# Performance work log

Hardware: AMD Instinct MI355X
Metric: run time of the kernel (lower is better)

## Reference

```python
import jax, jax.numpy as jnp
import numpy as np

H, CH, PQ, PV = 12, 16, 4, 8
C_S = 384
INF, EPS = 1e5, 1e-8
PT_W = -0.5


def setup_inputs() -> dict:
    key = jax.random.key(0)
    ks = jax.random.split(key, 20)
    B, C, N = 1, 8, 256
    s = jax.random.normal(ks[0], (B, C, N, C_S), jnp.float32)
    z = jax.random.normal(ks[1], (B, C, N, N, 8), jnp.float32)
    A = jax.random.normal(ks[2], (B, C, N, 3, 3), jnp.float32)
    rot = jnp.linalg.qr(A)[0]  # proper orthonormal frames
    trans = jax.random.normal(ks[3], (B, C, N, 3), jnp.float32) * 10.0
    mask = jnp.ones((B, C, N), jnp.float32)
    w = lambda k, i, o: jax.random.normal(k, (i, o), jnp.float32) * 0.02
    hc = H * CH
    return {
        's': s, 'z': z, 'rot': rot, 'trans': trans, 'mask': mask,
        'wq': w(ks[4], C_S, hc), 'bq': jnp.zeros((hc,)),
        'wkv': w(ks[5], C_S, 2 * hc), 'bkv': jnp.zeros((2 * hc,)),
        'g_gamma': jnp.ones((C_S,)), 'g_beta': jnp.zeros((C_S,)),
        'wgq': w(ks[6], C_S, hc), 'bgq': jnp.zeros((hc,)),
        'wgk': w(ks[7], C_S, hc), 'bgk': jnp.zeros((hc,)),
        'wqp': w(ks[8], C_S, H * PQ * 3), 'bqp': jnp.zeros((H * PQ * 3,)),
        'wkvp': w(ks[9], C_S, H * (PQ + PV) * 3), 'bkvp': jnp.zeros((H * (PQ + PV) * 3,)),
        'head_weights': jnp.full((H,), 0.5413248538970947, jnp.float32),  # softplus^-1(1)
        'wdist': w(ks[10], 1, H), 'bdist': jnp.zeros((H,)),
        'wout': w(ks[11], H * (CH + 4 * PV), C_S), 'bout': jnp.zeros((C_S,)),
    }


def _forward(s, z, rot, trans, mask, wq, bq, wkv, bkv, g_gamma, g_beta,
             wgq, bgq, wgk, bgk, wqp, bqp, wkvp, bkvp, head_weights,
             wdist, bdist, wout, bout):
    B, C, N, _ = s.shape
    q = (s @ wq + bq).reshape(B, C, N, H, CH)
    kv = (s @ wkv + bkv).reshape(B, C, N, H, 2 * CH)
    k, v = kv[..., :CH], kv[..., CH:]
    scale = (1.0 / (3 * CH)) ** 0.5
    a = jnp.einsum('bcihd,bcjhd->bchij', q, k) * scale  # [B,C,H,N,N]
    # global feature: mean over conformations, LayerNorm, QK bias
    s_g = s.mean(axis=-3)
    mu = s_g.mean(-1, keepdims=True)
    var = ((s_g - mu) ** 2).mean(-1, keepdims=True)
    s_gn = (s_g - mu) / jnp.sqrt(var + 1e-5) * g_gamma + g_beta
    g_q = (s_gn @ wgq + bgq).reshape(B, N, H, CH)
    g_k = (s_gn @ wgk + bgk).reshape(B, N, H, CH)
    a = a + jnp.einsum('bihd,bjhd->bhij', g_q, g_k)[:, None] * scale
    # invariant point attention term
    def to_pts(raw, P):
        pts = jnp.stack(jnp.split(raw, 3, axis=-1), axis=-1)  # [B,C,N,H*P,3]
        pts = jnp.einsum('bcnij,bcnpj->bcnpi', rot, pts) + trans[..., None, :]
        return pts.reshape(B, C, N, H, P, 3)
    q_pts = to_pts(s @ wqp + bqp, PQ)
    kv_pts = to_pts(s @ wkvp + bkvp, PQ + PV)
    k_pts, v_pts = kv_pts[..., :PQ, :], kv_pts[..., PQ:, :]
    diff2 = jnp.sum((q_pts[:, :, :, None] - k_pts[:, :, None]) ** 2, axis=-1)  # [B,C,N,N,H,PQ]
    hw = jax.nn.softplus(head_weights) * (1.0 / (3 * (PQ * 9.0 / 2))) ** 0.5
    pt_att = jnp.sum(diff2 * hw[:, None], axis=-1) * PT_W  # [B,C,N,N,H]
    a = a + jnp.moveaxis(pt_att, -1, -3)
    # mask
    sq_mask = mask[..., :, None] * mask[..., None, :]
    a = a + (INF * (sq_mask - 1.0))[..., None, :, :]
    # distance bias (torch uses a raw .view -> reshape, not transpose)
    dist = jnp.sqrt(jnp.sum((trans[..., :, None, :] - trans[..., None, :, :]) ** 2, axis=-1))
    db = dist[..., None] * wdist[0] + bdist  # [B,C,N,N,H]
    a = a + db.reshape(B, C, H, N, N)
    a = jax.nn.softmax(a, axis=-1)
    o = jnp.einsum('bchij,bcjhd->bcihd', a, v).reshape(B, C, N, H * CH)
    o_pt = jnp.einsum('bchij,bcjhpd->bcihpd', a, v_pts)  # [B,C,N,H,PV,3]
    o_pt = jnp.einsum('bcnji,bcnhpj->bcnhpi', rot, o_pt - trans[:, :, :, None, None, :])
    o_pt_norm = jnp.sqrt(jnp.sum(o_pt ** 2, axis=-1) + EPS).reshape(B, C, N, H * PV)
    o_pt_f = o_pt.reshape(B, C, N, H * PV, 3)
    feat = jnp.concatenate([o, o_pt_f[..., 0], o_pt_f[..., 1], o_pt_f[..., 2], o_pt_norm], axis=-1)
    return feat @ wout + bout, a


def reference(s, z, rot, trans, mask, wq, bq, wkv, bkv, g_gamma, g_beta,
              wgq, bgq, wgk, bgk, wqp, bqp, wkvp, bkvp, head_weights,
              wdist, bdist, wout, bout):
    return _forward(s, z, rot, trans, mask, wq, bq, wkv, bkv, g_gamma, g_beta,
                    wgq, bgq, wgk, bgk, wqp, bqp, wkvp, bkvp, head_weights,
                    wdist, bdist, wout, bout)
```

## Files before the change

### kernel.cpp

```cpp
#include <hip/hip_runtime.h>
#include <math.h>

#define NRES 256
#define CDIM 8
#define HNUM 12
#define CS   384

typedef __attribute__((ext_vector_type(8))) short bf16x8;
typedef __attribute__((ext_vector_type(4))) float f32x4;
typedef unsigned short ushort_t;

static __device__ __forceinline__ unsigned short f2bf(float x) {
    unsigned int u = __float_as_uint(x);
    unsigned int r = (u + 0x7fffu + ((u >> 16) & 1u)) >> 16;
    return (unsigned short)r;
}
static __device__ __forceinline__ float bf2f(unsigned short h) {
    return __uint_as_float(((unsigned int)h) << 16);
}

__global__ __launch_bounds__(256) void convert_kernel(
    const float* __restrict__ s,
    const float* __restrict__ wq, const float* __restrict__ bq,
    const float* __restrict__ wkv, const float* __restrict__ bkv,
    const float* __restrict__ wqp, const float* __restrict__ bqp,
    const float* __restrict__ wkvp, const float* __restrict__ bkvp,
    const float* __restrict__ wgq, const float* __restrict__ bgq,
    const float* __restrict__ wgk, const float* __restrict__ bgk,
    const float* __restrict__ wout,
    ushort_t* __restrict__ s_bf, ushort_t* __restrict__ wt_bf,
    ushort_t* __restrict__ wtg_bf, float* __restrict__ pbias,
    float* __restrict__ gbias,
    ushort_t* __restrict__ wo_hi, ushort_t* __restrict__ wo_lo)
{
    const int idx = blockIdx.x*256 + threadIdx.x;
    const int NS   = 2048*384;
    const int NWT  = 384*1152;
    const int NWTG = 384*384;
    const int NWO  = 576*384;
    if (idx < NS) {
        s_bf[idx] = f2bf(s[idx]);
    } else if (idx < NS + NWT) {
        const int t = idx - NS;
        const int k = t / 1152, vc = t - k*1152;
        const float* w; int C, lc;
        if (vc < 192)      { w = wq;   C = 192; lc = vc; }
        else if (vc < 576) { w = wkv;  C = 384; lc = vc - 192; }
        else if (vc < 720) { w = wqp;  C = 144; lc = vc - 576; }
        else               { w = wkvp; C = 432; lc = vc - 720; }
        wt_bf[(size_t)vc*384 + k] = f2bf(w[(size_t)k*C + lc]);
    } else if (idx < NS + NWT + NWTG) {
        const int t = idx - NS - NWT;
        const int k = t / 384, vc = t - k*384;
        const float val = (vc < 192) ? wgq[(size_t)k*192 + vc]
                                     : wgk[(size_t)k*192 + vc - 192];
        wtg_bf[(size_t)vc*384 + k] = f2bf(val);
    } else if (idx < NS + NWT + NWTG + 1152) {
        const int i = idx - NS - NWT - NWTG;
        float b;
        if (i < 192)      b = bq[i];
        else if (i < 576) b = bkv[i - 192];
        else if (i < 720) b = bqp[i - 576];
        else              b = bkvp[i - 720];
        pbias[i] = b;
    } else if (idx < NS + NWT + NWTG + 1152 + 384) {
        const int i = idx - NS - NWT - NWTG - 1152;
        gbias[i] = (i < 192) ? bgq[i] : bgk[i - 192];
    } else if (idx < NS + NWT + NWTG + 1536 + NWO) {
        const int t = idx - NS - NWT - NWTG - 1536;
        const int k = t / 384, n = t - k*384;
        const float wv = wout[t];
        const ushort_t hi = f2bf(wv);
        wo_hi[(size_t)n*576 + k] = hi;
        wo_lo[(size_t)n*576 + k] = f2bf(wv - bf2f(hi));
    }
}

__global__ __launch_bounds__(256) void proj_mfma_kernel(
    const ushort_t* __restrict__ s_bf, const ushort_t* __restrict__ wt_bf,
    const float* __restrict__ pbias,
    float* __restrict__ qo, float* __restrict__ ko, float* __restrict__ vo,
    float* __restrict__ rawp)
{
    const int blk = blockIdx.x;
    const int rt = blk / 18, ct = blk - rt*18;
    const int r0 = rt * 64, c0 = ct * 64;
    const int tid = threadIdx.x;
    const int wave = tid >> 6, lane = tid & 63;
    const int wrow = wave >> 1, wcol = wave & 1;
    const int m0 = r0 + wrow*32, n0 = c0 + wcol*32;
    const int qd = lane >> 4, lr = lane & 15;

    f32x4 acc00 = {0,0,0,0}, acc01 = {0,0,0,0}, acc10 = {0,0,0,0}, acc11 = {0,0,0,0};

    const ushort_t* a0p = s_bf  + (size_t)(m0 + lr)*384 + qd*8;
    const ushort_t* a1p = a0p + 16*384;
    const ushort_t* b0p = wt_bf + (size_t)(n0 + lr)*384 + qd*8;
    const ushort_t* b1p = b0p + 16*384;

    #pragma unroll
    for (int kk = 0; kk < 384; kk += 32) {
        const bf16x8 a0 = *(const bf16x8*)(a0p + kk);
        const bf16x8 a1 = *(const bf16x8*)(a1p + kk);
        const bf16x8 b0 = *(const bf16x8*)(b0p + kk);
        const bf16x8 b1 = *(const bf16x8*)(b1p + kk);
        acc00 = __builtin_amdgcn_mfma_f32_16x16x32_bf16(a0, b0, acc00, 0, 0, 0);
        acc01 = __builtin_amdgcn_mfma_f32_16x16x32_bf16(a0, b1, acc01, 0, 0, 0);
        acc10 = __builtin_amdgcn_mfma_f32_16x16x32_bf16(a1, b0, acc10, 0, 0, 0);
        acc11 = __builtin_amdgcn_mfma_f32_16x16x32_bf16(a1, b1, acc11, 0, 0, 0);
    }

    #pragma unroll
    for (int mt = 0; mt < 2; ++mt) {
        #pragma unroll
        for (int nt = 0; nt < 2; ++nt) {
            const f32x4 av = (mt==0) ? (nt==0 ? acc00 : acc01)
                                     : (nt==0 ? acc10 : acc11);
            const int col = n0 + nt*16 + lr;
            const float bb = pbias[col];
            #pragma unroll
            for (int reg = 0; reg < 4; ++reg) {
                const int row = m0 + mt*16 + qd*4 + reg;
                const float val = av[reg] + bb;
                if (col < 192) {
                    qo[(size_t)row*192 + col] = val;
                } else if (col < 576) {
                    const int lc = col - 192, h = lc >> 5, rm = lc & 31;
                    if (rm < 16) ko[(size_t)row*192 + h*16 + rm] = val;
                    else         vo[(size_t)row*192 + h*16 + rm - 16] = val;
                } else {
                    rawp[(size_t)row*576 + col - 576] = val;
                }
            }
        }
    }
}

__global__ __launch_bounds__(256) void pt_transform_kernel(
    const float* __restrict__ rawp, const float* __restrict__ rot,
    const float* __restrict__ trans,
    float* __restrict__ qpo, float* __restrict__ kpo, float* __restrict__ vpo)
{
    const int t = blockIdx.x*256 + threadIdx.x;
    const int row = t / 192;
    const int p = t - row*192;
    const float* R = rot + (size_t)row*9;
    const float* T = trans + (size_t)row*3;
    const float* base = rawp + (size_t)row*576;
    float x, y, z;
    if (p < 48) { x = base[p];       y = base[48+p];  z = base[96+p]; }
    else { const int pk = p-48; x = base[144+pk]; y = base[288+pk]; z = base[432+pk]; }
    const float px = R[0]*x + R[1]*y + R[2]*z + T[0];
    const float py = R[3]*x + R[4]*y + R[5]*z + T[1];
    const float pz = R[6]*x + R[7]*y + R[8]*z + T[2];
    if (p < 48) {
        float* o = qpo + (size_t)row*144 + p*3;
        o[0]=px; o[1]=py; o[2]=pz;
    } else {
        const int pk = p-48, h = pk/12, pp = pk - h*12;
        if (pp < 4) { float* o = kpo + (size_t)row*144 + (h*4+pp)*3;     o[0]=px; o[1]=py; o[2]=pz; }
        else        { float* o = vpo + (size_t)row*288 + (h*8+(pp-4))*3; o[0]=px; o[1]=py; o[2]=pz; }
    }
}

__global__ __launch_bounds__(256) void ln_kernel(
    const float* __restrict__ s, const float* __restrict__ g_gamma,
    const float* __restrict__ g_beta, ushort_t* __restrict__ sgn_bf)
{
    const int n = blockIdx.x;
    const int tid = threadIdx.x;
    __shared__ float sg[CS];
    __shared__ float red[256];

    for (int d = tid; d < CS; d += 256) {
        float acc = 0.f;
        for (int c = 0; c < CDIM; ++c) acc += s[((size_t)c*NRES+n)*CS + d];
        sg[d] = acc * (1.0f/CDIM);
    }
    __syncthreads();

    float lsum = 0.f;
    for (int d = tid; d < CS; d += 256) lsum += sg[d];
    red[tid] = lsum; __syncthreads();
    for (int st = 128; st > 0; st >>= 1) { if (tid < st) red[tid] += red[tid+st]; __syncthreads(); }
    const float mean = red[0] * (1.0f/CS);
    __syncthreads();

    float lvar = 0.f;
    for (int d = tid; d < CS; d += 256) { float df = sg[d]-mean; lvar += df*df; }
    red[tid] = lvar; __syncthreads();
    for (int st = 128; st > 0; st >>= 1) { if (tid < st) red[tid] += red[tid+st]; __syncthreads(); }
    const float var = red[0] * (1.0f/CS);
    __syncthreads();

    const float inv = rsqrtf(var + 1e-5f);
    for (int d = tid; d < CS; d += 256)
        sgn_bf[(size_t)n*CS + d] = f2bf((sg[d]-mean)*inv*g_gamma[d] + g_beta[d]);
}

__global__ __launch_bounds__(256) void ggemm_mfma_kernel(
    const ushort_t* __restrict__ sgn_bf, const ushort_t* __restrict__ wtg_bf,
    const float* __restrict__ gbias,
    float* __restrict__ gqo, float* __restrict__ gko)
{
    const int blk = blockIdx.x;
    const int rt = blk / 6, ct = blk - rt*6;
    const int r0 = rt * 64, c0 = ct * 64;
    const int tid = threadIdx.x;
    const int wave = tid >> 6, lane = tid & 63;
    const int wrow = wave >> 1, wcol = wave & 1;
    const int m0 = r0 + wrow*32, n0 = c0 + wcol*32;
    const int qd = lane >> 4, lr = lane & 15;

    f32x4 acc00 = {0,0,0,0}, acc01 = {0,0,0,0}, acc10 = {0,0,0,0}, acc11 = {0,0,0,0};

    const ushort_t* a0p = sgn_bf + (size_t)(m0 + lr)*384 + qd*8;
    const ushort_t* a1p = a0p + 16*384;
    const ushort_t* b0p = wtg_bf + (size_t)(n0 + lr)*384 + qd*8;
    const ushort_t* b1p = b0p + 16*384;

    #pragma unroll
    for (int kk = 0; kk < 384; kk += 32) {
        const bf16x8 a0 = *(const bf16x8*)(a0p + kk);
        const bf16x8 a1 = *(const bf16x8*)(a1p + kk);
        const bf16x8 b0 = *(const bf16x8*)(b0p + kk);
        const bf16x8 b1 = *(const bf16x8*)(b1p + kk);
        acc00 = __builtin_amdgcn_mfma_f32_16x16x32_bf16(a0, b0, acc00, 0, 0, 0);
        acc01 = __builtin_amdgcn_mfma_f32_16x16x32_bf16(a0, b1, acc01, 0, 0, 0);
        acc10 = __builtin_amdgcn_mfma_f32_16x16x32_bf16(a1, b0, acc10, 0, 0, 0);
        acc11 = __builtin_amdgcn_mfma_f32_16x16x32_bf16(a1, b1, acc11, 0, 0, 0);
    }

    #pragma unroll
    for (int mt = 0; mt < 2; ++mt) {
        #pragma unroll
        for (int nt = 0; nt < 2; ++nt) {
            const f32x4 av = (mt==0) ? (nt==0 ? acc00 : acc01)
                                     : (nt==0 ? acc10 : acc11);
            const int col = n0 + nt*16 + lr;
            const float bb = gbias[col];
            #pragma unroll
            for (int reg = 0; reg < 4; ++reg) {
                const int row = m0 + mt*16 + qd*4 + reg;
                const float val = av[reg] + bb;
                if (col < 192) gqo[(size_t)row*192 + col]       = val;
                else           gko[(size_t)row*192 + col - 192] = val;
            }
        }
    }
}

__global__ __launch_bounds__(256) void attn_mfma_kernel(
    const float* __restrict__ q, const float* __restrict__ k,
    const float* __restrict__ q_pts, const float* __restrict__ k_pts,
    const float* __restrict__ g_q, const float* __restrict__ g_k,
    const float* __restrict__ trans, const float* __restrict__ mask,
    const float* __restrict__ head_weights, const float* __restrict__ wdist,
    const float* __restrict__ bdist, float* __restrict__ a_out)
{
    const int blk  = blockIdx.x;
    const int half = blk & 1;
    const int ch   = blk >> 1;
    const int h    = ch % HNUM;
    const int c    = ch / HNUM;
    const int i0   = half * 128;
    const int tid  = threadIdx.x;

    __shared__ ushort_t Bsh[256*96];
    __shared__ ushort_t Ash[128*96];
    __shared__ float dsh[12*256];
    __shared__ float tsh[768];
    __shared__ float msh[256];
    __shared__ float kn_sh[256];
    __shared__ float qn_sh[128];
    __shared__ float wdsh[12], bdsh[12];
    __shared__ float cpart[96];
    __shared__ float censh[3];

    for (int t = tid; t < 768; t += 256) tsh[t] = trans[(size_t)c*768 + t];
    msh[tid] = mask[c*NRES + tid];
    if (tid < 12) { wdsh[tid] = wdist[tid]; bdsh[tid] = bdist[tid]; }
    __syncthreads();

    if (tid < 96) {
        const int coord = tid % 3, chunk = tid / 3;
        float sv = 0.f;
        for (int e = 0; e < 8; ++e) sv += tsh[(chunk*8+e)*3 + coord];
        cpart[tid] = sv;
    }
    __syncthreads();
    if (tid < 3) {
        float sv = 0.f;
        for (int e = 0; e < 32; ++e) sv += cpart[e*3 + tid];
        censh[tid] = sv * (1.0f/256.0f);
    }
    __syncthreads();

    const float s54   = 0.13608276348795434f;
    const float scale = 0.14433756729740643f;
    const float hwv = 0.5f * logf(1.0f + expf(head_weights[h])) * s54;
    const float sh  = sqrtf(2.0f * hwv);
    const float cx = censh[0], cy = censh[1], cz = censh[2];

    {
        const int j = tid;
        const float* kr  = k    + ((size_t)c*NRES + j)*192 + h*16;
        const float* gkr = g_k  + (size_t)j*192 + h*16;
        const float* kpr = k_pts+ ((size_t)c*NRES + j)*144 + h*12;
        ushort_t* br = &Bsh[j*96];
        #pragma unroll
        for (int e = 0; e < 16; ++e) br[e]    = f2bf(kr[e]);
        #pragma unroll
        for (int e = 0; e < 16; ++e) br[16+e] = f2bf(gkr[e]);
        float kn = 0.f;
        #pragma unroll
        for (int e = 0; e < 12; ++e) {
            const float cen = (e%3==0) ? cx : ((e%3==1) ? cy : cz);
            const float kp = kpr[e] - cen;
            kn += kp*kp;
            const float sp = sh * kp;
            const ushort_t hi = f2bf(sp);
            br[32+e] = hi;
            br[44+e] = f2bf(sp - bf2f(hi));
            br[56+e] = hi;
        }
        #pragma unroll
        for (int e = 68; e < 96; ++e) br[e] = 0;
        kn_sh[j] = hwv * kn;
    }

    if (tid < 128) {
        const int il = i0 + tid;
        const float* qr  = q    + ((size_t)c*NRES + il)*192 + h*16;
        const float* gqr = g_q  + (size_t)il*192 + h*16;
        const float* qpr = q_pts+ ((size_t)c*NRES + il)*144 + h*12;
        ushort_t* ar = &Ash[tid*96];
        #pragma unroll
        for (int e = 0; e < 16; ++e) ar[e]    = f2bf(scale*qr[e]);
        #pragma unroll
        for (int e = 0; e < 16; ++e) ar[16+e] = f2bf(scale*gqr[e]);
        float qn = 0.f;
        #pragma unroll
        for (int e = 0; e < 12; ++e) {
            const float cen = (e%3==0) ? cx : ((e%3==1) ? cy : cz);
            const float qp = qpr[e] - cen;
            qn += qp*qp;
            const float sp = sh * qp;
            const ushort_t hi = f2bf(sp);
            ar[32+e] = hi;
            ar[44+e] = hi;
            ar[56+e] = f2bf(sp - bf2f(hi));
        }
        #pragma unroll
        for (int e = 68; e < 96; ++e) ar[e] = 0;
        qn_sh[tid] = hwv * qn;
    }

    const int Fmin = h*65536 + i0*256;
    const int iibase = Fmin / 3072;
    const int NI = (Fmin + 127*256 + 255)/3072 - iibase + 1;
    for (int idx = tid; idx < NI*256; idx += 256) {
        const int e = idx >> 8, jj = idx & 255;
        const int ia = iibase + e;
        const float dx = tsh[ia*3+0] - tsh[jj*3+0];
        const float dy = tsh[ia*3+1] - tsh[jj*3+1];
        const float dz = tsh[ia*3+2] - tsh[jj*3+2];
        dsh[idx] = sqrtf(dx*dx + dy*dy + dz*dz);
    }
    __syncthreads();

    const int wave = tid >> 6, lane = tid & 63;
    const int qd = lane >> 4, lr = lane & 15;

    for (int g = 0; g < 2; ++g) {
        const int m0 = wave*32 + g*16;
        const ushort_t* ap = &Ash[(m0 + lr)*96 + qd*8];
        const bf16x8 af0 = *(const bf16x8*)(ap);
        const bf16x8 af1 = *(const bf16x8*)(ap + 32);
        const bf16x8 af2 = *(const bf16x8*)(ap + 64);

        f32x4 acc[16];
        #pragma unroll
        for (int t = 0; t < 16; ++t) {
            const ushort_t* bp = &Bsh[(t*16 + lr)*96 + qd*8];
            f32x4 a = {0.f,0.f,0.f,0.f};
            a = __builtin_amdgcn_mfma_f32_16x16x32_bf16(af0, *(const bf16x8*)(bp),      a, 0, 0, 0);
            a = __builtin_amdgcn_mfma_f32_16x16x32_bf16(af1, *(const bf16x8*)(bp + 32), a, 0, 0, 0);
            a = __builtin_amdgcn_mfma_f32_16x16x32_bf16(af2, *(const bf16x8*)(bp + 64), a, 0, 0, 0);
            acc[t] = a;
        }

        const int ibase = m0 + qd*4;
        float qn_r[4], mb_r[4];
        int F0_[4];
        #pragma unroll
        for (int r = 0; r < 4; ++r) {
            const int il = i0 + ibase + r;
            qn_r[r] = qn_sh[ibase + r];
            mb_r[r] = 100000.0f * msh[il];
            F0_[r]  = h*65536 + il*256;
        }

        float mx[4] = {-1e30f,-1e30f,-1e30f,-1e30f};
        #pragma unroll
        for (int t = 0; t < 16; ++t) {
            const int j = t*16 + lr;
            const float knj = kn_sh[j];
            const float mj  = msh[j];
            #pragma unroll
            for (int r = 0; r < 4; ++r) {
                const unsigned int f = (unsigned int)(F0_[r] + j);
                const unsigned int p = f / 12u;
                const int ho = (int)(f - p*12u);
                const int ii = (int)(p >> 8);
                const int jj = (int)(p & 255u);
                const float dist = dsh[(ii - iibase)*256 + jj];
                const float db = dist*wdsh[ho] + bdsh[ho];
                const float lv = acc[t][r] - qn_r[r] - knj
                               + (mb_r[r]*mj - 100000.0f) + db;
                acc[t][r] = lv;
                mx[r] = fmaxf(mx[r], lv);
            }
        }
        #pragma unroll
        for (int r = 0; r < 4; ++r) {
            #pragma unroll
            for (int off = 1; off < 16; off <<= 1)
                mx[r] = fmaxf(mx[r], __shfl_xor(mx[r], off));
        }
        float sm[4] = {0.f,0.f,0.f,0.f};
        #pragma unroll
        for (int t = 0; t < 16; ++t) {
            #pragma unroll
            for (int r = 0; r < 4; ++r) {
                const float e = __expf(acc[t][r] - mx[r]);
                acc[t][r] = e;
                sm[r] += e;
            }
        }
        #pragma unroll
        for (int r = 0; r < 4; ++r) {
            #pragma unroll
            for (int off = 1; off < 16; off <<= 1)
                sm[r] += __shfl_xor(sm[r], off);
            sm[r] = 1.0f / sm[r];
        }
        float* dst = a_out + ((size_t)ch*NRES + (i0 + ibase))*NRES;
        #pragma unroll
        for (int t = 0; t < 16; ++t) {
            #pragma unroll
            for (int r = 0; r < 4; ++r)
                dst[(size_t)r*NRES + t*16 + lr] = acc[t][r]*sm[r];
        }
    }
}

#define ASTRB 264
__global__ __launch_bounds__(256) void out_feat_mfma_kernel(
    const float* __restrict__ a, const float* __restrict__ v,
    const float* __restrict__ v_pts, const float* __restrict__ rot,
    const float* __restrict__ trans,
    ushort_t* __restrict__ feat_hi, ushort_t* __restrict__ feat_lo)
{
    const int blk = blockIdx.x;
    const int qtr = blk & 3;
    const int ch  = blk >> 2;
    const int h   = ch % HNUM;
    const int c   = ch / HNUM;
    const int i0  = qtr * 64;
    const int tid = threadIdx.x;

    __shared__ ushort_t Bt[64*ASTRB];
    __shared__ float opt[64*25];
    __shared__ float osh[64*17];
    __shared__ float cpart[96];
    __shared__ float censh[3];

    if (tid < 96) {
        const int coord = tid % 3, chunk = tid / 3;
        float sv = 0.f;
        for (int e = 0; e < 8; ++e)
            sv += trans[((size_t)c*NRES + chunk*8 + e)*3 + coord];
        cpart[tid] = sv;
    }
    __syncthreads();
    if (tid < 3) {
        float sv = 0.f;
        for (int e = 0; e < 32; ++e) sv += cpart[e*3 + tid];
        censh[tid] = sv * (1.0f/256.0f);
    }
    __syncthreads();
    const float cx = censh[0], cy = censh[1], cz = censh[2];
    const float cen3[3] = {cx, cy, cz};

    {
        const int j = tid;
        const float4* vr = (const float4*)(v + ((size_t)c*NRES + j)*192 + h*16);
        #pragma unroll
        for (int e4 = 0; e4 < 4; ++e4) {
            const float4 w = vr[e4];
            Bt[(e4*4+0)*ASTRB + j] = f2bf(w.x);
            Bt[(e4*4+1)*ASTRB + j] = f2bf(w.y);
            Bt[(e4*4+2)*ASTRB + j] = f2bf(w.z);
            Bt[(e4*4+3)*ASTRB + j] = f2bf(w.w);
        }
        const float4* vpr = (const float4*)(v_pts + ((size_t)c*NRES + j)*288 + h*24);
        #pragma unroll
        for (int e4 = 0; e4 < 6; ++e4) {
            const float4 w = vpr[e4];
            const float vals[4] = {w.x, w.y, w.z, w.w};
            #pragma unroll
            for (int cc = 0; cc < 4; ++cc) {
                const int e = e4*4 + cc;
                const float vp = vals[cc] - cen3[e % 3];
                const ushort_t hi = f2bf(vp);
                Bt[(16+e)*ASTRB + j] = hi;
                Bt[(40+e)*ASTRB + j] = f2bf(vp - bf2f(hi));
            }
        }
    }
    __syncthreads();

    const int wave = tid >> 6, lane = tid & 63;
    const int qd = lane >> 4, lr = lane & 15;
    const int m0 = wave*16;

    const float* arow = a + ((size_t)ch*NRES + i0 + m0 + lr)*NRES;

    f32x4 acc[4] = {{0,0,0,0},{0,0,0,0},{0,0,0,0},{0,0,0,0}};
    #pragma unroll
    for (int kk = 0; kk < 256; kk += 32) {
        const float4 a0 = *(const float4*)(arow + qd*8 + kk);
        const float4 a1 = *(const float4*)(arow + qd*8 + kk + 4);
        const float av[8] = {a0.x,a0.y,a0.z,a0.w,a1.x,a1.y,a1.z,a1.w};
        bf16x8 ahi, alo;
        #pragma unroll
        for (int e = 0; e < 8; ++e) {
            const ushort_t hi = f2bf(av[e]);
            ((ushort_t*)&ahi)[e] = hi;
            ((ushort_t*)&alo)[e] = f2bf(av[e] - bf2f(hi));
        }
        #pragma unroll
        for (int t = 0; t < 4; ++t) {
            const bf16x8 bf = *(const bf16x8*)&Bt[(t*16 + lr)*ASTRB + qd*8 + kk];
            acc[t] = __builtin_amdgcn_mfma_f32_16x16x32_bf16(ahi, bf, acc[t], 0, 0, 0);
            acc[t] = __builtin_amdgcn_mfma_f32_16x16x32_bf16(alo, bf, acc[t], 0, 0, 0);
        }
    }

    #pragma unroll
    for (int reg = 0; reg < 4; ++reg) {
        const int row_l = m0 + qd*4 + reg;
        osh[row_l*17 + lr] = acc[0][reg];
        opt[row_l*25 + lr] = acc[1][reg];
    }
    #pragma unroll
    for (int reg = 0; reg < 4; ++reg) {
        const int row_l = m0 + qd*4 + reg;
        if (lr < 8) opt[row_l*25 + 16 + lr] = acc[2][reg];
        else        opt[row_l*25 + (lr-8)] += acc[2][reg];
    }
    #pragma unroll
    for (int reg = 0; reg < 4; ++reg) {
        const int row_l = m0 + qd*4 + reg;
        opt[row_l*25 + 8 + lr] += acc[3][reg];
    }
    __syncthreads();

    #pragma unroll
    for (int it = 0; it < 4; ++it) {
        const int idx = it*256 + tid;
        const int row_l = idx >> 4, e = idx & 15;
        const int grow = c*NRES + i0 + row_l;
        const float val = osh[row_l*17 + e];
        const ushort_t hi = f2bf(val);
        feat_hi[(size_t)grow*576 + h*16 + e] = hi;
        feat_lo[(size_t)grow*576 + h*16 + e] = f2bf(val - bf2f(hi));
    }
    #pragma unroll
    for (int it = 0; it < 2; ++it) {
        const int idx = it*256 + tid;
        const int row_l = idx >> 3, p = idx & 7;
        const int grow = c*NRES + i0 + row_l;
        const float* R = rot + (size_t)grow*9;
        const float* T = trans + (size_t)grow*3;
        const float x = opt[row_l*25 + p*3+0] + cx - T[0];
        const float y = opt[row_l*25 + p*3+1] + cy - T[1];
        const float z = opt[row_l*25 + p*3+2] + cz - T[2];
        const float rx = R[0]*x + R[3]*y + R[6]*z;
        const float ry = R[1]*x + R[4]*y + R[7]*z;
        const float rz = R[2]*x + R[5]*y + R[8]*z;
        const float nm = sqrtf(rx*rx + ry*ry + rz*rz + 1e-8f);
        const float vals[4] = {rx, ry, rz, nm};
        #pragma unroll
        for (int sl = 0; sl < 4; ++sl) {
            const int col = 192 + sl*96 + h*8 + p;
            const ushort_t hi = f2bf(vals[sl]);
            feat_hi[(size_t)grow*576 + col] = hi;
            feat_lo[(size_t)grow*576 + col] = f2bf(vals[sl] - bf2f(hi));
        }
    }
}

__global__ __launch_bounds__(256) void out_gemm_mfma_kernel(
    const ushort_t* __restrict__ feat_hi, const ushort_t* __restrict__ feat_lo,
    const ushort_t* __restrict__ wo_hi, const ushort_t* __restrict__ wo_lo,
    const float* __restrict__ bout, float* __restrict__ out0)
{
    const int blk = blockIdx.x;
    const int rt = blk / 6, ct = blk - rt*6;
    const int r0 = rt * 64, c0 = ct * 64;
    const int tid = threadIdx.x;
    const int wave = tid >> 6, lane = tid & 63;
    const int wrow = wave >> 1, wcol = wave & 1;
    const int m0 = r0 + wrow*32, n0 = c0 + wcol*32;
    const int qd = lane >> 4, lr = lane & 15;

    f32x4 acc[2][2] = {{{0,0,0,0},{0,0,0,0}},{{0,0,0,0},{0,0,0,0}}};

    const ushort_t* ah0 = feat_hi + (size_t)(m0 + lr)*576 + qd*8;
    const ushort_t* ah1 = ah0 + 16*576;
    const ushort_t* al0 = feat_lo + (size_t)(m0 + lr)*576 + qd*8;
    const ushort_t* al1 = al0 + 16*576;
    const ushort_t* bh0 = wo_hi + (size_t)(n0 + lr)*576 + qd*8;
    const ushort_t* bh1 = bh0 + 16*576;
    const ushort_t* bl0 = wo_lo + (size_t)(n0 + lr)*576 + qd*8;
    const ushort_t* bl1 = bl0 + 16*576;

    for (int kk = 0; kk < 576; kk += 32) {
        const bf16x8 fh0 = *(const bf16x8*)(ah0 + kk);
        const bf16x8 fh1 = *(const bf16x8*)(ah1 + kk);
        const bf16x8 fl0 = *(const bf16x8*)(al0 + kk);
        const bf16x8 fl1 = *(const bf16x8*)(al1 + kk);
        const bf16x8 wh0 = *(const bf16x8*)(bh0 + kk);
        const bf16x8 wh1 = *(const bf16x8*)(bh1 + kk);
        const bf16x8 wl0 = *(const bf16x8*)(bl0 + kk);
        const bf16x8 wl1 = *(const bf16x8*)(bl1 + kk);
        acc[0][0] = __builtin_amdgcn_mfma_f32_16x16x32_bf16(fh0, wh0, acc[0][0], 0, 0, 0);
        acc[0][1] = __builtin_amdgcn_mfma_f32_16x16x32_bf16(fh0, wh1, acc[0][1], 0, 0, 0);
        acc[1][0] = __builtin_amdgcn_mfma_f32_16x16x32_bf16(fh1, wh0, acc[1][0], 0, 0, 0);
        acc[1][1] = __builtin_amdgcn_mfma_f32_16x16x32_bf16(fh1, wh1, acc[1][1], 0, 0, 0);
        acc[0][0] = __builtin_amdgcn_mfma_f32_16x16x32_bf16(fl0, wh0, acc[0][0], 0, 0, 0);
        acc[0][1] = __builtin_amdgcn_mfma_f32_16x16x32_bf16(fl0, wh1, acc[0][1], 0, 0, 0);
        acc[1][0] = __builtin_amdgcn_mfma_f32_16x16x32_bf16(fl1, wh0, acc[1][0], 0, 0, 0);
        acc[1][1] = __builtin_amdgcn_mfma_f32_16x16x32_bf16(fl1, wh1, acc[1][1], 0, 0, 0);
        acc[0][0] = __builtin_amdgcn_mfma_f32_16x16x32_bf16(fh0, wl0, acc[0][0], 0, 0, 0);
        acc[0][1] = __builtin_amdgcn_mfma_f32_16x16x32_bf16(fh0, wl1, acc[0][1], 0, 0, 0);
        acc[1][0] = __builtin_amdgcn_mfma_f32_16x16x32_bf16(fh1, wl0, acc[1][0], 0, 0, 0);
        acc[1][1] = __builtin_amdgcn_mfma_f32_16x16x32_bf16(fh1, wl1, acc[1][1], 0, 0, 0);
    }

    #pragma unroll
    for (int mt = 0; mt < 2; ++mt) {
        #pragma unroll
        for (int nt = 0; nt < 2; ++nt) {
            const int col = n0 + nt*16 + lr;
            const float bb = bout[col];
            #pragma unroll
            for (int reg = 0; reg < 4; ++reg) {
                const int row = m0 + mt*16 + qd*4 + reg;
                out0[(size_t)row*CS + col] = acc[mt][nt][reg] + bb;
            }
        }
    }
}

extern "C" void kernel_launch(void* const* d_in, const int* in_sizes, int n_in,
                              void* d_out, int out_size, void* d_ws, size_t ws_size,
                              hipStream_t stream)
{
    const float* s     = (const float*)d_in[0];
    const float* rot   = (const float*)d_in[2];
    const float* trans = (const float*)d_in[3];
    const float* mask  = (const float*)d_in[4];
    const float* wq    = (const float*)d_in[5];
    const float* bq    = (const float*)d_in[6];
    const float* wkv   = (const float*)d_in[7];
    const float* bkv   = (const float*)d_in[8];
    const float* g_gamma = (const float*)d_in[9];
    const float* g_beta  = (const float*)d_in[10];
    const float* wgq   = (const float*)d_in[11];
    const float* bgq   = (const float*)d_in[12];
    const float* wgk   = (const float*)d_in[13];
    const float* bgk   = (const float*)d_in[14];
    const float* wqp   = (const float*)d_in[15];
    const float* bqp   = (const float*)d_in[16];
    const float* wkvp  = (const float*)d_in[17];
    const float* bkvp  = (const float*)d_in[18];
    const float* head_weights = (const float*)d_in[19];
    const float* wdist = (const float*)d_in[20];
    const float* bdist = (const float*)d_in[21];
    const float* wout  = (const float*)d_in[22];
    const float* bout  = (const float*)d_in[23];

    float* ws      = (float*)d_ws;
    float* q_buf   = ws + 0;
    float* qp_buf  = ws + 393216;
    float* kp_buf  = ws + 688128;
    float* gq_buf  = ws + 983040;
    float* gk_buf  = ws + 1032192;
    float* k_buf   = ws + 1081344;
    float* v_buf   = ws + 1474560;
    float* vp_buf  = ws + 1867776;
    ushort_t* sgn_bf  = (ushort_t*)(ws + 1867776);
    ushort_t* feat_hi = (ushort_t*)(ws + 2457600);
    ushort_t* feat_lo = (ushort_t*)(ws + 3047424);
    ushort_t* wo_hi   = (ushort_t*)(ws + 3637248);
    ushort_t* wo_lo   = (ushort_t*)(ws + 3747840);

    float* out0  = (float*)d_out;
    float* a_out = out0 + 786432;
    float*    rawp   = a_out;
    ushort_t* s_bf   = (ushort_t*)(a_out + 1179648);
    ushort_t* wt_bf  = (ushort_t*)(a_out + 1572864);
    ushort_t* wtg_bf = (ushort_t*)(a_out + 1794048);
    float*    pbias  = a_out + 1867776;
    float*    gbias  = a_out + 1868928;

    convert_kernel<<<6246, 256, 0, stream>>>(s, wq, bq, wkv, bkv, wqp, bqp,
                                             wkvp, bkvp, wgq, bgq, wgk, bgk, wout,
                                             s_bf, wt_bf, wtg_bf, pbias, gbias,
                                             wo_hi, wo_lo);
    ln_kernel<<<256, 256, 0, stream>>>(s, g_gamma, g_beta, sgn_bf);
    proj_mfma_kernel<<<576, 256, 0, stream>>>(s_bf, wt_bf, pbias,
                                              q_buf, k_buf, v_buf, rawp);
    ggemm_mfma_kernel<<<24, 256, 0, stream>>>(sgn_bf, wtg_bf, gbias,
                                              gq_buf, gk_buf);
    pt_transform_kernel<<<1536, 256, 0, stream>>>(rawp, rot, trans,
                                                  qp_buf, kp_buf, vp_buf);
    attn_mfma_kernel<<<192, 256, 0, stream>>>(q_buf, k_buf, qp_buf, kp_buf,
                                              gq_buf, gk_buf, trans, mask,
                                              head_weights, wdist, bdist, a_out);
    out_feat_mfma_kernel<<<384, 256, 0, stream>>>(a_out, v_buf, vp_buf, rot, trans,
                                                  feat_hi, feat_lo);
    out_gemm_mfma_kernel<<<192, 256, 0, stream>>>(feat_hi, feat_lo, wo_hi, wo_lo,
                                                  bout, out0);
}
```

Baseline: 219.3 us.

## Split attention into quarter-row blocks, pad LDS stride, vectorize loads, truncate hi/lo splits

The attention kernel now uses 64-row quarters instead of 128-row halves, doubling the grid to 384 blocks to fill more CUs. Each wave handles one 16-row tile. The LDS row stride is padded from 96 to 104 to reduce bank conflicts, and Q/K loads use float4. The trans staging array is dropped in favour of direct global reads. Throughout the file, round-to-nearest bf16 hi/lo splitting is replaced by truncation masking, which is cheaper and keeps hi+lo accuracy. The cost is redundant K-side staging per block and uncached global reads of trans.

```diff
diff --git a/kernel.cpp b/kernel.cpp
--- a/kernel.cpp
+++ b/kernel.cpp
@@ -70,9 +70,10 @@
         const int t = idx - NS - NWT - NWTG - 1536;
         const int k = t / 384, n = t - k*384;
         const float wv = wout[t];
-        const ushort_t hi = f2bf(wv);
-        wo_hi[(size_t)n*576 + k] = hi;
-        wo_lo[(size_t)n*576 + k] = f2bf(wv - bf2f(hi));
+        const unsigned int u = __float_as_uint(wv);
+        const float hif = __uint_as_float(u & 0xFFFF0000u);
+        wo_hi[(size_t)n*576 + k] = (ushort_t)(u >> 16);
+        wo_lo[(size_t)n*576 + k] = (ushort_t)(__float_as_uint(wv - hif) >> 16);
     }
 }
 
@@ -250,6 +251,7 @@
     }
 }
 
+#define BSTR 104
 __global__ __launch_bounds__(256) void attn_mfma_kernel(
     const float* __restrict__ q, const float* __restrict__ k,
     const float* __restrict__ q_pts, const float* __restrict__ k_pts,
@@ -259,33 +261,31 @@
     const float* __restrict__ bdist, float* __restrict__ a_out)
 {
     const int blk  = blockIdx.x;
-    const int half = blk & 1;
-    const int ch   = blk >> 1;
+    const int qtr  = blk & 3;
+    const int ch   = blk >> 2;
     const int h    = ch % HNUM;
     const int c    = ch / HNUM;
-    const int i0   = half * 128;
+    const int i0   = qtr * 64;
     const int tid  = threadIdx.x;
 
-    __shared__ ushort_t Bsh[256*96];
-    __shared__ ushort_t Ash[128*96];
-    __shared__ float dsh[12*256];
-    __shared__ float tsh[768];
+    __shared__ ushort_t Bsh[256*BSTR];
+    __shared__ ushort_t Ash[64*BSTR];
+    __shared__ float dsh[7*256];
     __shared__ float msh[256];
     __shared__ float kn_sh[256];
-    __shared__ float qn_sh[128];
+    __shared__ float qn_sh[64];
     __shared__ float wdsh[12], bdsh[12];
     __shared__ float cpart[96];
     __shared__ float censh[3];
 
-    for (int t = tid; t < 768; t += 256) tsh[t] = trans[(size_t)c*768 + t];
     msh[tid] = mask[c*NRES + tid];
     if (tid < 12) { wdsh[tid] = wdist[tid]; bdsh[tid] = bdist[tid]; }
-    __syncthreads();
 
     if (tid < 96) {
         const int coord = tid % 3, chunk = tid / 3;
         float sv = 0.f;
-        for (int e = 0; e < 8; ++e) sv += tsh[(chunk*8+e)*3 + coord];
+        for (int e = 0; e < 8; ++e)
+            sv += trans[((size_t)c*NRES + chunk*8 + e)*3 + coord];
         cpart[tid] = sv;
     }
     __syncthreads();
@@ -301,27 +301,43 @@
     const float hwv = 0.5f * logf(1.0f + expf(head_weights[h])) * s54;
     const float sh  = sqrtf(2.0f * hwv);
     const float cx = censh[0], cy = censh[1], cz = censh[2];
+    const float cen3[3] = {cx, cy, cz};
 
     {
         const int j = tid;
-        const float* kr  = k    + ((size_t)c*NRES + j)*192 + h*16;
-        const float* gkr = g_k  + (size_t)j*192 + h*16;
-        const float* kpr = k_pts+ ((size_t)c*NRES + j)*144 + h*12;
-        ushort_t* br = &Bsh[j*96];
-        #pragma unroll
-        for (int e = 0; e < 16; ++e) br[e]    = f2bf(kr[e]);
-        #pragma unroll
-        for (int e = 0; e < 16; ++e) br[16+e] = f2bf(gkr[e]);
+        const float4* kr4 = (const float4*)(k    + ((size_t)c*NRES + j)*192 + h*16);
+        const float4* gk4 = (const float4*)(g_k  + (size_t)j*192 + h*16);
+        const float4* kp4 = (const float4*)(k_pts+ ((size_t)c*NRES + j)*144 + h*12);
+        ushort_t* br = &Bsh[j*BSTR];
+        #pragma unroll
+        for (int e4 = 0; e4 < 4; ++e4) {
+            const float4 w = kr4[e4];
+            br[e4*4+0] = f2bf(w.x); br[e4*4+1] = f2bf(w.y);
+            br[e4*4+2] = f2bf(w.z); br[e4*4+3] = f2bf(w.w);
+        }
+        #pragma unroll
+        for (int e4 = 0; e4 < 4; ++e4) {
+            const float4 w = gk4[e4];
+            br[16+e4*4+0] = f2bf(w.x); br[16+e4*4+1] = f2bf(w.y);
+            br[16+e4*4+2] = f2bf(w.z); br[16+e4*4+3] = f2bf(w.w);
+        }
+        float kp_a[12];
+        #pragma unroll
+        for (int e4 = 0; e4 < 3; ++e4) {
+            const float4 w = kp4[e4];
+            kp_a[e4*4+0]=w.x; kp_a[e4*4+1]=w.y; kp_a[e4*4+2]=w.z; kp_a[e4*4+3]=w.w;
+        }
         float kn = 0.f;
         #pragma unroll
         for (int e = 0; e < 12; ++e) {
-            const float cen = (e%3==0) ? cx : ((e%3==1) ? cy : cz);
-            const float kp = kpr[e] - cen;
+            const float kp = kp_a[e] - cen3[e % 3];
             kn += kp*kp;
             const float sp = sh * kp;
-            const ushort_t hi = f2bf(sp);
+            const unsigned int u = __float_as_uint(sp);
+            const float hif = __uint_as_float(u & 0xFFFF0000u);
+            const ushort_t hi = (ushort_t)(u >> 16);
             br[32+e] = hi;
-            br[44+e] = f2bf(sp - bf2f(hi));
+            br[44+e] = (ushort_t)(__float_as_uint(sp - hif) >> 16);
             br[56+e] = hi;
         }
         #pragma unroll
@@ -329,27 +345,42 @@
         kn_sh[j] = hwv * kn;
     }
 
-    if (tid < 128) {
+    if (tid < 64) {
         const int il = i0 + tid;
-        const float* qr  = q    + ((size_t)c*NRES + il)*192 + h*16;
-        const float* gqr = g_q  + (size_t)il*192 + h*16;
-        const float* qpr = q_pts+ ((size_t)c*NRES + il)*144 + h*12;
-        ushort_t* ar = &Ash[tid*96];
-        #pragma unroll
-        for (int e = 0; e < 16; ++e) ar[e]    = f2bf(scale*qr[e]);
-        #pragma unroll
-        for (int e = 0; e < 16; ++e) ar[16+e] = f2bf(scale*gqr[e]);
+        const float4* qr4 = (const float4*)(q    + ((size_t)c*NRES + il)*192 + h*16);
+        const float4* gq4 = (const float4*)(g_q  + (size_t)il*192 + h*16);
+        const float4* qp4 = (const float4*)(q_pts+ ((size_t)c*NRES + il)*144 + h*12);
+        ushort_t* ar = &Ash[tid*BSTR];
+        #pragma unroll
+        for (int e4 = 0; e4 < 4; ++e4) {
+            const float4 w = qr4[e4];
+            ar[e4*4+0] = f2bf(scale*w.x); ar[e4*4+1] = f2bf(scale*w.y);
+            ar[e4*4+2] = f2bf(scale*w.z); ar[e4*4+3] = f2bf(scale*w.w);
+        }
+        #pragma unroll
+        for (int e4 = 0; e4 < 4; ++e4) {
+            const float4 w = gq4[e4];
+            ar[16+e4*4+0] = f2bf(scale*w.x); ar[16+e4*4+1] = f2bf(scale*w.y);
+            ar[16+e4*4+2] = f2bf(scale*w.z); ar[16+e4*4+3] = f2bf(scale*w.w);
+        }
+        float qp_a[12];
+        #pragma unroll
+        for (int e4 = 0; e4 < 3; ++e4) {
+            const float4 w = qp4[e4];
+            qp_a[e4*4+0]=w.x; qp_a[e4*4+1]=w.y; qp_a[e4*4+2]=w.z; qp_a[e4*4+3]=w.w;
+        }
         float qn = 0.f;
         #pragma unroll
         for (int e = 0; e < 12; ++e) {
-            const float cen = (e%3==0) ? cx : ((e%3==1) ? cy : cz);
-            const float qp = qpr[e] - cen;
+            const float qp = qp_a[e] - cen3[e % 3];
             qn += qp*qp;
             const float sp = sh * qp;
-            const ushort_t hi = f2bf(sp);
+            const unsigned int u = __float_as_uint(sp);
+            const float hif = __uint_as_float(u & 0xFFFF0000u);
+            const ushort_t hi = (ushort_t)(u >> 16);
             ar[32+e] = hi;
             ar[44+e] = hi;
-            ar[56+e] = f2bf(sp - bf2f(hi));
+            ar[56+e] = (ushort_t)(__float_as_uint(sp - hif) >> 16);
         }
         #pragma unroll
         for (int e = 68; e < 96; ++e) ar[e] = 0;
@@ -358,100 +389,99 @@
 
     const int Fmin = h*65536 + i0*256;
     const int iibase = Fmin / 3072;
-    const int NI = (Fmin + 127*256 + 255)/3072 - iibase + 1;
+    const int NI = (Fmin + 63*256 + 255)/3072 - iibase + 1;
+    const float* tch = trans + (size_t)c*768;
     for (int idx = tid; idx < NI*256; idx += 256) {
         const int e = idx >> 8, jj = idx & 255;
         const int ia = iibase + e;
-        const float dx = tsh[ia*3+0] - tsh[jj*3+0];
-        const float dy = tsh[ia*3+1] - tsh[jj*3+1];
-        const float dz = tsh[ia*3+2] - tsh[jj*3+2];
+        const float dx = tch[ia*3+0] - tch[jj*3+0];
+        const float dy = tch[ia*3+1] - tch[jj*3+1];
+        const float dz = tch[ia*3+2] - tch[jj*3+2];
         dsh[idx] = sqrtf(dx*dx + dy*dy + dz*dz);
     }
     __syncthreads();
 
     const int wave = tid >> 6, lane = tid & 63;
     const int qd = lane >> 4, lr = lane & 15;
-
-    for (int g = 0; g < 2; ++g) {
-        const int m0 = wave*32 + g*16;
-        const ushort_t* ap = &Ash[(m0 + lr)*96 + qd*8];
-        const bf16x8 af0 = *(const bf16x8*)(ap);
-        const bf16x8 af1 = *(const bf16x8*)(ap + 32);
-        const bf16x8 af2 = *(const bf16x8*)(ap + 64);
-
-        f32x4 acc[16];
-        #pragma unroll
-        for (int t = 0; t < 16; ++t) {
-            const ushort_t* bp = &Bsh[(t*16 + lr)*96 + qd*8];
-            f32x4 a = {0.f,0.f,0.f,0.f};
-            a = __builtin_amdgcn_mfma_f32_16x16x32_bf16(af0, *(const bf16x8*)(bp),      a, 0, 0, 0);
-            a = __builtin_amdgcn_mfma_f32_16x16x32_bf16(af1, *(const bf16x8*)(bp + 32), a, 0, 0, 0);
-            a = __builtin_amdgcn_mfma_f32_16x16x32_bf16(af2, *(const bf16x8*)(bp + 64), a, 0, 0, 0);
-            acc[t] = a;
-        }
-
-        const int ibase = m0 + qd*4;
-        float qn_r[4], mb_r[4];
-        int F0_[4];
+    const int m0 = wave*16;
+
+    const ushort_t* ap = &Ash[(m0 + lr)*BSTR + qd*8];
+    const bf16x8 af0 = *(const bf16x8*)(ap);
+    const bf16x8 af1 = *(const bf16x8*)(ap + 32);
+    const bf16x8 af2 = *(const bf16x8*)(ap + 64);
+
+    f32x4 acc[16];
+    #pragma unroll
+    for (int t = 0; t < 16; ++t) {
+        const ushort_t* bp = &Bsh[(t*16 + lr)*BSTR + qd*8];
+        f32x4 a = {0.f,0.f,0.f,0.f};
+        a = __builtin_amdgcn_mfma_f32_16x16x32_bf16(af0, *(const bf16x8*)(bp),      a, 0, 0, 0);
+        a = __builtin_amdgcn_mfma_f32_16x16x32_bf16(af1, *(const bf16x8*)(bp + 32), a, 0, 0, 0);
+        a = __builtin_amdgcn_mfma_f32_16x16x32_bf16(af2, *(const bf16x8*)(bp + 64), a, 0, 0, 0);
+        acc[t] = a;
+    }
+
+    const int ibase = m0 + qd*4;
+    float qn_r[4], mb_r[4];
+    int F0_[4];
+    #pragma unroll
+    for (int r = 0; r < 4; ++r) {
+        const int il = i0 + ibase + r;
+        qn_r[r] = qn_sh[ibase + r];
+        mb_r[r] = 100000.0f * msh[il];
+        F0_[r]  = h*65536 + il*256;
+    }
+
+    float mx[4] = {-1e30f,-1e30f,-1e30f,-1e30f};
+    #pragma unroll
+    for (int t = 0; t < 16; ++t) {
+        const int j = t*16 + lr;
+        const float knj = kn_sh[j];
+        const float mj  = msh[j];
         #pragma unroll
         for (int r = 0; r < 4; ++r) {
-            const int il = i0 + ibase + r;
-            qn_r[r] = qn_sh[ibase + r];
-            mb_r[r] = 100000.0f * msh[il];
-            F0_[r]  = h*65536 + il*256;
-        }
-
-        float mx[4] = {-1e30f,-1e30f,-1e30f,-1e30f};
-        #pragma unroll
-        for (int t = 0; t < 16; ++t) {
-            const int j = t*16 + lr;
-            const float knj = kn_sh[j];
-            const float mj  = msh[j];
-            #pragma unroll
-            for (int r = 0; r < 4; ++r) {
-                const unsigned int f = (unsigned int)(F0_[r] + j);
-                const unsigned int p = f / 12u;
-                const int ho = (int)(f - p*12u);
-                const int ii = (int)(p >> 8);
-                const int jj = (int)(p & 255u);
-                const float dist = dsh[(ii - iibase)*256 + jj];
-                const float db = dist*wdsh[ho] + bdsh[ho];
-                const float lv = acc[t][r] - qn_r[r] - knj
-                               + (mb_r[r]*mj - 100000.0f) + db;
-                acc[t][r] = lv;
-                mx[r] = fmaxf(mx[r], lv);
-            }
-        }
+            const unsigned int f = (unsigned int)(F0_[r] + j);
+            const unsigned int p = f / 12u;
+            const int ho = (int)(f - p*12u);
+            const int ii = (int)(p >> 8);
+            const int jj = (int)(p & 255u);
+            const float dist = dsh[(ii - iibase)*256 + jj];
+            const float db = dist*wdsh[ho] + bdsh[ho];
+            const float lv = acc[t][r] - qn_r[r] - knj
+                           + (mb_r[r]*mj - 100000.0f) + db;
+            acc[t][r] = lv;
+            mx[r] = fmaxf(mx[r], lv);
+        }
+    }
+    #pragma unroll
+    for (int r = 0; r < 4; ++r) {
+        #pragma unroll
+        for (int off = 1; off < 16; off <<= 1)
+            mx[r] = fmaxf(mx[r], __shfl_xor(mx[r], off));
+    }
+    float sm[4] = {0.f,0.f,0.f,0.f};
+    #pragma unroll
+    for (int t = 0; t < 16; ++t) {
         #pragma unroll
         for (int r = 0; r < 4; ++r) {
-            #pragma unroll
-            for (int off = 1; off < 16; off <<= 1)
-                mx[r] = fmaxf(mx[r], __shfl_xor(mx[r], off));
-        }
-        float sm[4] = {0.f,0.f,0.f,0.f};
-        #pragma unroll
-        for (int t = 0; t < 16; ++t) {
-            #pragma unroll
-            for (int r = 0; r < 4; ++r) {
-                const float e = __expf(acc[t][r] - mx[r]);
-                acc[t][r] = e;
-                sm[r] += e;
-            }
-        }
-        #pragma unroll
-        for (int r = 0; r < 4; ++r) {
-            #pragma unroll
-            for (int off = 1; off < 16; off <<= 1)
-                sm[r] += __shfl_xor(sm[r], off);
-            sm[r] = 1.0f / sm[r];
-        }
-        float* dst = a_out + ((size_t)ch*NRES + (i0 + ibase))*NRES;
-        #pragma unroll
-        for (int t = 0; t < 16; ++t) {
-            #pragma unroll
-            for (int r = 0; r < 4; ++r)
-                dst[(size_t)r*NRES + t*16 + lr] = acc[t][r]*sm[r];
-        }
+            const float e = __expf(acc[t][r] - mx[r]);
+            acc[t][r] = e;
+            sm[r] += e;
+        }
+    }
+    #pragma unroll
+    for (int r = 0; r < 4; ++r) {
+        #pragma unroll
+        for (int off = 1; off < 16; off <<= 1)
+            sm[r] += __shfl_xor(sm[r], off);
+        sm[r] = 1.0f / sm[r];
+    }
+    float* dst = a_out + ((size_t)ch*NRES + (i0 + ibase))*NRES;
+    #pragma unroll
+    for (int t = 0; t < 16; ++t) {
+        #pragma unroll
+        for (int r = 0; r < 4; ++r)
+            dst[(size_t)r*NRES + t*16 + lr] = acc[t][r]*sm[r];
     }
 }
 
@@ -513,9 +543,10 @@
             for (int cc = 0; cc < 4; ++cc) {
                 const int e = e4*4 + cc;
                 const float vp = vals[cc] - cen3[e % 3];
-                const ushort_t hi = f2bf(vp);
-                Bt[(16+e)*ASTRB + j] = hi;
-                Bt[(40+e)*ASTRB + j] = f2bf(vp - bf2f(hi));
+                const unsigned int u = __float_as_uint(vp);
+                const float hif = __uint_as_float(u & 0xFFFF0000u);
+                Bt[(16+e)*ASTRB + j] = (ushort_t)(u >> 16);
+                Bt[(40+e)*ASTRB + j] = (ushort_t)(__float_as_uint(vp - hif) >> 16);
             }
         }
     }
@@ -536,9 +567,10 @@
         bf16x8 ahi, alo;
         #pragma unroll
         for (int e = 0; e < 8; ++e) {
-            const ushort_t hi = f2bf(av[e]);
-            ((ushort_t*)&ahi)[e] = hi;
-            ((ushort_t*)&alo)[e] = f2bf(av[e] - bf2f(hi));
+            const unsigned int u = __float_as_uint(av[e]);
+            const float hif = __uint_as_float(u & 0xFFFF0000u);
+            ((ushort_t*)&ahi)[e] = (ushort_t)(u >> 16);
+            ((ushort_t*)&alo)[e] = (ushort_t)(__float_as_uint(av[e] - hif) >> 16);
         }
         #pragma unroll
         for (int t = 0; t < 4; ++t) {
@@ -573,9 +605,10 @@
         const int row_l = idx >> 4, e = idx & 15;
         const int grow = c*NRES + i0 + row_l;
         const float val = osh[row_l*17 + e];
-        const ushort_t hi = f2bf(val);
-        feat_hi[(size_t)grow*576 + h*16 + e] = hi;
-        feat_lo[(size_t)grow*576 + h*16 + e] = f2bf(val - bf2f(hi));
+        const unsigned int u = __float_as_uint(val);
+        const float hif = __uint_as_float(u & 0xFFFF0000u);
+        feat_hi[(size_t)grow*576 + h*16 + e] = (ushort_t)(u >> 16);
+        feat_lo[(size_t)grow*576 + h*16 + e] = (ushort_t)(__float_as_uint(val - hif) >> 16);
     }
     #pragma unroll
     for (int it = 0; it < 2; ++it) {
@@ -595,9 +628,11 @@
         #pragma unroll
         for (int sl = 0; sl < 4; ++sl) {
             const int col = 192 + sl*96 + h*8 + p;
-            const ushort_t hi = f2bf(vals[sl]);
-            feat_hi[(size_t)grow*576 + col] = hi;
-            feat_lo[(size_t)grow*576 + col] = f2bf(vals[sl] - bf2f(hi));
+            const float vv = vals[sl];
+            const unsigned int u = __float_as_uint(vv);
+            const float hif = __uint_as_float(u & 0xFFFF0000u);
+            feat_hi[(size_t)grow*576 + col] = (ushort_t)(u >> 16);
+            feat_lo[(size_t)grow*576 + col] = (ushort_t)(__float_as_uint(vv - hif) >> 16);
         }
     }
 }
@@ -728,7 +763,7 @@
                                               gq_buf, gk_buf);
     pt_transform_kernel<<<1536, 256, 0, stream>>>(rawp, rot, trans,
                                                   qp_buf, kp_buf, vp_buf);
-    attn_mfma_kernel<<<192, 256, 0, stream>>>(q_buf, k_buf, qp_buf, kp_buf,
+    attn_mfma_kernel<<<384, 256, 0, stream>>>(q_buf, k_buf, qp_buf, kp_buf,
                                               gq_buf, gk_buf, trans, mask,
                                               head_weights, wdist, bdist, a_out);
     out_feat_mfma_kernel<<<384, 256, 0, stream>>>(a_out, v_buf, vp_buf, rot, trans,
```

Result: faster. 211.9 us (-3.4%).
